# Kernel optimization log

Hardware: AMD Instinct MI355X
Metric: run time of the kernel (lower is better)

The kernel has to match this reference:

```python
import jax, jax.numpy as jnp
import numpy as np

N_COUNTRIES = 8
ADJ = jnp.array([
    [0, 1, 1, 1, 1, 1, 1, 0],
    [1, 0, 1, 0, 0, 0, 0, 1],
    [1, 1, 0, 1, 0, 1, 0, 0],
    [1, 0, 1, 0, 1, 1, 1, 0],
    [1, 0, 0, 1, 0, 1, 1, 0],
    [1, 0, 1, 1, 1, 0, 0, 0],
    [1, 0, 0, 1, 1, 0, 0, 0],
    [0, 1, 0, 0, 0, 0, 0, 0]], dtype=jnp.float32)
GDP = jnp.array([0.4, 0.15, 0.12, 0.1, 0.08, 0.08, 0.05, 0.02], dtype=jnp.float32)

B, D_IN, H, NH, L = 8192, 512, 256, 4, 3
HD = H * NH  # 1024: QKV width (no head reshape in the original)


def layer_norm(x, g, b, eps=1e-5):
    m = x.mean(-1, keepdims=True)
    v = ((x - m) ** 2).mean(-1, keepdims=True)
    return (x - m) * jax.lax.rsqrt(v + eps) * g + b


def setup_inputs() -> dict:
    key = jax.random.key(0)
    ks = jax.random.split(key, 12)
    lin = lambda k, i, o: (jax.random.normal(k, (i, o), jnp.float32) / np.sqrt(i).astype(np.float32))
    lin3 = lambda k, i, o: (jax.random.normal(k, (L, i, o), jnp.float32) / np.sqrt(i).astype(np.float32))
    return {
        'regional_features': jax.random.normal(ks[0], (B, D_IN), jnp.float32),
        'Wi': lin(ks[1], D_IN, H), 'bi': jnp.zeros((H,), jnp.float32),
        'emb': 0.02 * jax.random.normal(ks[2], (N_COUNTRIES, H), jnp.float32),
        'Wq': lin3(ks[3], H, HD), 'bq': jnp.zeros((L, HD), jnp.float32),
        'Wk': lin3(ks[4], H, HD), 'bk': jnp.zeros((L, HD), jnp.float32),
        'Wv': lin3(ks[5], H, HD), 'bv': jnp.zeros((L, HD), jnp.float32),
        'Wo': lin3(ks[6], HD, H), 'bo': jnp.zeros((L, H), jnp.float32),
        'ln_g': jnp.ones((L, H), jnp.float32), 'ln_b': jnp.zeros((L, H), jnp.float32),
        'Wp': lin(ks[7], H, H), 'bp': jnp.zeros((H,), jnp.float32),
        'lnp_g': jnp.ones((H,), jnp.float32), 'lnp_b': jnp.zeros((H,), jnp.float32),
    }


def reference(regional_features, Wi, bi, emb, Wq, bq, Wk, bk, Wv, bv, Wo, bo,
              ln_g, ln_b, Wp, bp, lnp_g, lnp_b):
    # input projection + broadcast over the 8 countries + country embedding
    h = regional_features @ Wi + bi                     # [B, H]
    x = h[:, None, :] + emb[None, :, :]                 # [B, 8, H]
    scale = 1.0 / np.sqrt(H).astype(np.float32)         # sqrt(dim)=sqrt(256), as in original
    mask = ADJ == 0                                     # [8, 8]
    for l in range(L):
        Q = x @ Wq[l] + bq[l]                           # [B, 8, HD]
        K = x @ Wk[l] + bk[l]
        V = x @ Wv[l] + bv[l]
        scores = jnp.einsum('bnd,bmd->bnm', Q, K) * scale  # [B, 8, 8]
        scores = jnp.where(mask[None], -jnp.inf, scores)
        attn = jax.nn.softmax(scores, axis=-1)          # dropout is identity in eval
        out = jnp.einsum('bnm,bmd->bnd', attn, V)       # [B, 8, HD]
        out = out @ Wo[l] + bo[l]                       # [B, 8, H]
        x = layer_norm(x + out, ln_g[l], ln_b[l])
    regional = jnp.sum(x * GDP[None, :, None], axis=1)  # [B, H]
    p = layer_norm(regional @ Wp + bp, lnp_g, lnp_b)
    return jax.nn.gelu(p, approximate=False)            # torch nn.GELU default = exact erf
```

## Files before the change

kernel.cpp:

```cpp
#include <hip/hip_runtime.h>
#include <hip/hip_bf16.h>
#include <math.h>


typedef short bf16x8 __attribute__((ext_vector_type(8)));
typedef float f32x4  __attribute__((ext_vector_type(4)));

__device__ __forceinline__ float bflo(unsigned int u){ return __uint_as_float(u << 16); }
__device__ __forceinline__ float bfhi(unsigned int u){ return __uint_as_float(u & 0xffff0000u); }
__device__ __forceinline__ float bfs(short s){ return __uint_as_float((unsigned int)(unsigned short)s << 16); }
__device__ __forceinline__ unsigned short f2bf(float f){
  __hip_bfloat16 h = __float2bfloat16(f);
  return *reinterpret_cast<unsigned short*>(&h);
}
__device__ __forceinline__ int gsw(int r, int q){ return (r + 16*q) ^ (r >> 2); }
__device__ __forceinline__ void unpack8(uint4 a, float* o){
  o[0]=bflo(a.x); o[1]=bfhi(a.x); o[2]=bflo(a.y); o[3]=bfhi(a.y);
  o[4]=bflo(a.z); o[5]=bfhi(a.z); o[6]=bflo(a.w); o[7]=bfhi(a.w);
}
__device__ __forceinline__ uint4 pack8(const float* v){
  uint4 r;
  r.x = (unsigned int)f2bf(v[0]) | ((unsigned int)f2bf(v[1]) << 16);
  r.y = (unsigned int)f2bf(v[2]) | ((unsigned int)f2bf(v[3]) << 16);
  r.z = (unsigned int)f2bf(v[4]) | ((unsigned int)f2bf(v[5]) << 16);
  r.w = (unsigned int)f2bf(v[6]) | ((unsigned int)f2bf(v[7]) << 16);
  return r;
}
__device__ __forceinline__ void gload16(const void* g, void* l){
  __builtin_amdgcn_global_load_lds(
      (const __attribute__((address_space(1))) unsigned int*)g,
      (__attribute__((address_space(3))) unsigned int*)l, 16, 0, 0);
}
__device__ __forceinline__ bf16x8 shfl8(bf16x8 v, int src){
  union U { bf16x8 h; int u[4]; };
  U a, r; a.h = v;
  #pragma unroll
  for (int j = 0; j < 4; j++) r.u[j] = __shfl(a.u[j], src);
  return r.h;
}
__device__ __forceinline__ bf16x8 pk8(const float* v){
  bf16x8 r;
  #pragma unroll
  for (int j = 0; j < 8; j++) r[j] = (short)f2bf(v[j]);
  return r;
}

struct CvP { const float* src[4]; short* dst[4]; int boff[5]; };
__global__ __launch_bounds__(256) void k_convert(CvP p){
  int bid = blockIdx.x, s = 0;
  while (bid >= p.boff[s+1]) s++;
  size_t e = (size_t)(bid - p.boff[s]) * 2048 + (size_t)threadIdx.x * 8;
  const float* src = p.src[s] + e;
  float4 v0 = *(const float4*)src;
  float4 v1 = *(const float4*)(src + 4);
  float v[8] = {v0.x,v0.y,v0.z,v0.w,v1.x,v1.y,v1.z,v1.w};
  *(uint4*)(p.dst[s] + e) = pack8(v);
}

struct TrP { const float* src[5]; short* dst[5]; int rows[5]; int cols[5]; int toff[6]; };
__global__ __launch_bounds__(256) void k_transpose(TrP p){
  __shared__ float tile[64][65];
  int bid = blockIdx.x, s = 0;
  while (bid >= p.toff[s+1]) s++;
  int ti = bid - p.toff[s];
  int cols = p.cols[s], rows = p.rows[s];
  int ntc = cols >> 6;
  int r0 = (ti / ntc) * 64, c0 = (ti % ntc) * 64;
  const float* src = p.src[s];
  int row = threadIdx.x >> 2, jb = (threadIdx.x & 3) * 16;
  #pragma unroll
  for (int j = 0; j < 16; j += 4){
    float4 v = *(const float4*)(src + (size_t)(r0 + row) * cols + c0 + jb + j);
    tile[row][jb+j] = v.x; tile[row][jb+j+1] = v.y; tile[row][jb+j+2] = v.z; tile[row][jb+j+3] = v.w;
  }
  __syncthreads();
  short* dst = p.dst[s];
  float tmp[16];
  #pragma unroll
  for (int j = 0; j < 16; j++) tmp[j] = tile[jb + j][row];
  #pragma unroll
  for (int j = 0; j < 16; j += 8)
    *(uint4*)(dst + (size_t)(c0 + row) * rows + r0 + jb + j) = pack8(&tmp[j]);
}

__global__ __launch_bounds__(256) void k_vecs2(
    const short* Wqb, const short* Wkb, const short* WoTb,
    const float* bq, const float* bk, const float* bv, const float* bo,
    float* cq, float* ck, float* cvo, float* c0){
  const int job = blockIdx.x, l = blockIdx.y, tid = threadIdx.x;
  __shared__ float sv[1024];
  __shared__ float red[256];
  if (job == 3){
    float pp = 0.f;
    #pragma unroll
    for (int i = 0; i < 4; i++){
      int d = tid*4 + i;
      pp = fmaf(bq[l*1024 + d], bk[l*1024 + d], pp);
    }
    red[tid] = pp; __syncthreads();
    for (int o = 128; o > 0; o >>= 1){ if (tid < o) red[tid] += red[tid + o]; __syncthreads(); }
    if (tid == 0) c0[l] = red[0] * 0.0625f;
    return;
  }
  const short* rows = (job==0 ? Wqb : job==1 ? Wkb : WoTb) + (size_t)l*262144;
  const float* vecg = (job==0 ? bk : job==1 ? bq : bv) + l*1024;
  const float scale = (job == 2) ? 1.0f : 0.0625f;
  for (int i = tid; i < 1024; i += 256) sv[i] = vecg[i];
  __syncthreads();
  const int row = tid >> 3, sub = tid & 7;
  for (int pass = 0; pass < 8; pass++){
    int r = pass*32 + row;
    const short* rp = rows + (size_t)r*1024;
    float acc = 0.f;
    #pragma unroll
    for (int i = 0; i < 16; i++){
      int d = sub*8 + i*64;
      uint4 v = *(const uint4*)(rp + d);
      float f[8]; unpack8(v, f);
      #pragma unroll
      for (int j = 0; j < 8; j++) acc = fmaf(f[j], sv[d + j], acc);
    }
    acc += __shfl_xor(acc, 1); acc += __shfl_xor(acc, 2); acc += __shfl_xor(acc, 4);
    if (sub == 0){
      float o = acc * scale;
      if (job == 2) o += bo[l*256 + r];
      (job==0 ? cq : job==1 ? ck : cvo)[l*256 + r] = o;
    }
  }
}

struct GDesc { const short* A; const short* Bt; short* C; int K; float scale; };
struct GemmP { GDesc d[6]; };
__global__ __launch_bounds__(256) void k_gemm128(GemmP p){
  GDesc g = p.d[blockIdx.z];
  const int tid = threadIdx.x, lane = tid & 63, w = tid >> 6;
  const int wm = w >> 1, wn = w & 1;
  __shared__ alignas(16) short As[128*32];
  __shared__ alignas(16) short Bs[128*32];
  const int K = g.K;
  const short* Ab = g.A + (size_t)blockIdx.x * 128 * K;
  const short* Bb = g.Bt + (size_t)blockIdx.y * 128 * K;
  f32x4 acc[4][4] = {};
  for (int k0 = 0; k0 < K; k0 += 32){
    #pragma unroll
    for (int i = 0; i < 2; i++){
      int s = w*2 + i;
      int ro = (s >> 2)*64 + (s & 3)*16 + (lane & 15);
      int co = k0 + (lane >> 4) * 8;
      gload16(Ab + (size_t)ro * K + co, &As[s*512]);
      gload16(Bb + (size_t)ro * K + co, &Bs[s*512]);
    }
    __syncthreads();
    bf16x8 av[4], bv[4];
    #pragma unroll
    for (int mi = 0; mi < 4; mi++)
      av[mi] = *(const bf16x8*)&As[((wm*4 + mi)*64 + lane)*8];
    #pragma unroll
    for (int nj = 0; nj < 4; nj++)
      bv[nj] = *(const bf16x8*)&Bs[((wn*4 + nj)*64 + lane)*8];
    #pragma unroll
    for (int mi = 0; mi < 4; mi++)
      #pragma unroll
      for (int nj = 0; nj < 4; nj++)
        acc[mi][nj] = __builtin_amdgcn_mfma_f32_16x16x32_bf16(av[mi], bv[nj], acc[mi][nj], 0, 0, 0);
    __syncthreads();
  }
  const int ldc = gridDim.y * 128;
  #pragma unroll
  for (int mi = 0; mi < 4; mi++)
    #pragma unroll
    for (int nj = 0; nj < 4; nj++){
      int rm0 = blockIdx.x*128 + wm*64 + mi*16 + (lane >> 4) * 4;
      int cn  = blockIdx.y*128 + wn*64 + nj*16 + (lane & 15);
      #pragma unroll
      for (int j = 0; j < 4; j++)
        g.C[(size_t)(rm0 + j) * ldc + cn] = (short)f2bf(acc[mi][nj][j] * g.scale);
    }
}

struct RpP { const short* src[8]; short* dst[8]; int K[8]; int boff[9]; };
__global__ __launch_bounds__(256) void k_repack(RpP p){
  int bid = blockIdx.x, s = 0;
  while (bid >= p.boff[s+1]) s++;
  int kk = bid - p.boff[s];
  const short* src = p.src[s];
  short* dst = p.dst[s] + (size_t)kk * 8192;
  int K = p.K[s];
  int r15 = threadIdx.x & 15, nt = threadIdx.x >> 4;
  const short* sp = src + (size_t)(nt*16 + r15) * K + kk*32;
  short* dp = dst + nt*512 + r15*8;
  #pragma unroll
  for (int q = 0; q < 4; q++)
    *(uint4*)(dp + q*128) = *(const uint4*)(sp + q*8);
}

__global__ __launch_bounds__(512, 2) void k_net(
    const float* __restrict__ rf, const short* __restrict__ WiT,
    const float* __restrict__ bi, const float* __restrict__ emb,
    const short* __restrict__ Wqk, const short* __restrict__ Wvo,
    const float* __restrict__ ckv, const float* __restrict__ cvov,
    const float* __restrict__ lng, const float* __restrict__ lnb,
    const short* __restrict__ WpT, const float* __restrict__ bpv,
    const float* __restrict__ lpg, const float* __restrict__ lpb,
    float* __restrict__ outp){
  const int tid = threadIdx.x, lane = tid & 63, w = tid >> 6;
  const int b0 = blockIdx.x * 16;
  const int dsub = (lane >> 4) * 8;
  const int glane = gsw(lane & 15, lane >> 4);
  __shared__ alignas(16) short tst[8][4096];
  __shared__ alignas(16) short wbuf[32768];
  __shared__ alignas(16) float atn[8][16][16];
  __shared__ short ckb[256];
  __shared__ float s_add[256], s_g[256], s_b[256];
  __shared__ float redS[8][16], redQ[8][16], s_mean[16], s_rstd[16];

  #define LKW  asm volatile("s_waitcnt lgkmcnt(0)" ::: "memory")
  #define VMW0 asm volatile("s_waitcnt vmcnt(0)" ::: "memory")

  auto STAGEW = [&](const short* W, int h){
    #pragma unroll
    for (int i = 0; i < 8; i++)
      gload16(W + (size_t)(w*16 + h*8 + i)*512 + lane*8, &wbuf[(w*8 + i)*512]);
  };

  float* hst  = (float*)&tst[0][0];
  float* embs = hst + 16*264;
  float* bis  = embs + 2048;
  if (tid < 256) bis[tid] = bi[tid];
  for (int i = tid; i < 2048; i += 512) embs[i] = emb[i];
  f32x4 hacc[2] = {};
  #pragma unroll
  for (int kk = 0; kk < 16; kk++){
    const float* ap = rf + (size_t)(b0 + (lane & 15)) * 512 + kk*32 + dsub;
    float4 a0 = *(const float4*)ap, a1 = *(const float4*)(ap + 4);
    float af[8] = {a0.x,a0.y,a0.z,a0.w,a1.x,a1.y,a1.z,a1.w};
    bf16x8 av = pk8(af);
    #pragma unroll
    for (int nj = 0; nj < 2; nj++){
      bf16x8 bv = *(const bf16x8*)(WiT + (size_t)(kk*16 + w*2 + nj)*512 + lane*8);
      hacc[nj] = __builtin_amdgcn_mfma_f32_16x16x32_bf16(av, bv, hacc[nj], 0, 0, 0);
    }
  }
  __syncthreads();
  #pragma unroll
  for (int nj = 0; nj < 2; nj++)
    #pragma unroll
    for (int jj = 0; jj < 4; jj++){
      int m = (lane >> 4)*4 + jj, col = w*32 + nj*16 + (lane & 15);
      hst[m*264 + col] = hacc[nj][jj] + bis[col];
    }
  __syncthreads();
  bf16x8 xf[8];
  {
    int r15 = lane & 15;
    int bt = w*2 + (r15 >> 3), ct = r15 & 7;
    #pragma unroll
    for (int c = 0; c < 8; c++){
      float v8[8];
      #pragma unroll
      for (int e = 0; e < 8; e++){
        int d = dsub + 32*c + e;
        v8[e] = hst[bt*264 + d] + embs[ct*256 + d];
      }
      xf[c] = pk8(v8);
    }
  }

  const unsigned long long MASK64 = 0x02191D69752B857EULL;

  #pragma unroll 1
  for (int l = 0; l < 3; ++l){
    __syncthreads();
    if (tid < 256){
      ckb[tid]   = (short)f2bf(ckv[l*256 + tid]);
      s_add[tid] = cvov[l*256 + tid];
      s_g[tid]   = lng[l*256 + tid];
      s_b[tid]   = lnb[l*256 + tid];
    }
    const short* Wq_ = Wqk + l*65536;
    const short* Wv_ = Wvo + l*65536;
    STAGEW(Wq_, 0);
    VMW0; __syncthreads();

    f32x4 sacc = {0.f, 0.f, 0.f, 0.f};
    #pragma unroll
    for (int h = 0; h < 2; h++){
      f32x4 acc[8] = {};
      #pragma unroll
      for (int kk = 0; kk < 8; kk++)
        #pragma unroll
        for (int nj = 0; nj < 8; nj++){
          bf16x8 bv = *(const bf16x8*)&wbuf[(kk*8 + nj)*512 + lane*8];
          acc[nj] = __builtin_amdgcn_mfma_f32_16x16x32_bf16(xf[kk], bv, acc[nj], 0, 0, 0);
        }
      if (h == 0){ __syncthreads(); STAGEW(Wq_, 1); }
      #pragma unroll
      for (int nj = 0; nj < 8; nj++)
        #pragma unroll
        for (int jj = 0; jj < 4; jj++){
          int i_ = (lane >> 4)*4 + jj, nl = nj*16 + (lane & 15);
          tst[w][(nl >> 5)*512 + gsw(i_, (nl >> 3) & 3)*8 + (nl & 7)] = (short)f2bf(acc[nj][jj]);
        }
      LKW; __builtin_amdgcn_sched_barrier(0);
      #pragma unroll
      for (int cl = 0; cl < 4; cl++){
        bf16x8 tf = *(const bf16x8*)&tst[w][cl*512 + glane*8];
        sacc = __builtin_amdgcn_mfma_f32_16x16x32_bf16(tf, xf[h*4 + cl], sacc, 0, 0, 0);
      }
      LKW;
      if (h == 0){ VMW0; __syncthreads(); }
    }
    __syncthreads();
    STAGEW(Wv_, 0);

    float skv = 0.f;
    #pragma unroll
    for (int c = 0; c < 8; c++){
      bf16x8 cv = *(const bf16x8*)&ckb[c*32 + dsub];
      #pragma unroll
      for (int e = 0; e < 8; e++) skv = fmaf(bfs(xf[c][e]), bfs(cv[e]), skv);
    }
    skv += __shfl_xor(skv, 16); skv += __shfl_xor(skv, 32);

    #pragma unroll
    for (int jj = 0; jj < 4; jj++){
      int i_ = (lane >> 4)*4 + jj, j_ = lane & 15;
      bool ok = (((i_ ^ j_) & 8) == 0) &&
                ((MASK64 >> (((i_ & 7) << 3) | (j_ & 7))) & 1ull);
      float sv = ok ? (sacc[jj] + skv) : -3.0e38f;
      float mx = sv;
      mx = fmaxf(mx, __shfl_xor(mx, 1));
      mx = fmaxf(mx, __shfl_xor(mx, 2));
      mx = fmaxf(mx, __shfl_xor(mx, 4));
      float e = ok ? __expf(sv - mx) : 0.f;
      float sum = e;
      sum += __shfl_xor(sum, 1); sum += __shfl_xor(sum, 2); sum += __shfl_xor(sum, 4);
      atn[w][i_][j_] = e / sum;
    }
    LKW;

    bf16x8 yfrag[8];
    {
      float4 A0 = *(const float4*)&atn[w][lane & 15][lane & 8];
      float4 A1 = *(const float4*)&atn[w][lane & 15][(lane & 8) + 4];
      float am[8] = {A0.x, A0.y, A0.z, A0.w, A1.x, A1.y, A1.z, A1.w};
      #pragma unroll
      for (int c = 0; c < 8; c++){
        float a8[8] = {0,0,0,0,0,0,0,0};
        #pragma unroll
        for (int mi = 0; mi < 8; mi++){
          bf16x8 xs = shfl8(xf[c], (lane & 48) | (lane & 8) | mi);
          #pragma unroll
          for (int e = 0; e < 8; e++) a8[e] = fmaf(am[mi], bfs(xs[e]), a8[e]);
        }
        yfrag[c] = pk8(a8);
      }
    }
    VMW0; __syncthreads();

    float rs = 0.f, rq = 0.f;
    float* fst = (float*)&tst[w][0];
    #pragma unroll
    for (int h = 0; h < 2; h++){
      f32x4 acc[8] = {};
      #pragma unroll
      for (int kk = 0; kk < 8; kk++)
        #pragma unroll
        for (int nj = 0; nj < 8; nj++){
          bf16x8 bv = *(const bf16x8*)&wbuf[(kk*8 + nj)*512 + lane*8];
          acc[nj] = __builtin_amdgcn_mfma_f32_16x16x32_bf16(yfrag[kk], bv, acc[nj], 0, 0, 0);
        }
      if (h == 0){ __syncthreads(); STAGEW(Wv_, 1); }
      #pragma unroll
      for (int nj = 0; nj < 8; nj++)
        #pragma unroll
        for (int jj = 0; jj < 4; jj++){
          int i_ = (lane >> 4)*4 + jj;
          int dq = nj*16 + (lane & 15);
          fst[(dq >> 5)*512 + gsw(i_, (dq >> 3) & 3)*8 + (dq & 7)] = acc[nj][jj];
        }
      LKW; __builtin_amdgcn_sched_barrier(0);
      #pragma unroll
      for (int lc = 0; lc < 4; lc++){
        int c = h*4 + lc;
        float v8[8];
        #pragma unroll
        for (int e = 0; e < 8; e++){
          int d = 32*c + dsub + e;
          float t = fst[lc*512 + glane*8 + e] + s_add[d] + bfs(xf[c][e]);
          rs += t; rq = fmaf(t, t, rq);
          v8[e] = t;
        }
        xf[c] = pk8(v8);
      }
      LKW;
      if (h == 0){ VMW0; __syncthreads(); }
    }
    rs += __shfl_xor(rs, 16); rs += __shfl_xor(rs, 32);
    rq += __shfl_xor(rq, 16); rq += __shfl_xor(rq, 32);
    float mn = rs * (1.f/256.f);
    float var = rq * (1.f/256.f) - mn*mn;
    float rr = rsqrtf(fmaxf(var, 0.f) + 1e-5f);
    #pragma unroll
    for (int c = 0; c < 8; c++){
      float v8[8];
      #pragma unroll
      for (int e = 0; e < 8; e++){
        int d = 32*c + dsub + e;
        v8[e] = (bfs(xf[c][e]) - mn) * rr * s_g[d] + s_b[d];
      }
      xf[c] = pk8(v8);
    }
  }

  __syncthreads();
  short* Ast = &tst[0][0];
  {
    int c7 = lane & 7;
    float g = (c7 == 0) ? 0.4f : (c7 == 1) ? 0.15f : (c7 == 2) ? 0.12f :
              (c7 == 3) ? 0.1f : (c7 == 4) ? 0.08f : (c7 == 5) ? 0.08f :
              (c7 == 6) ? 0.05f : 0.02f;
    #pragma unroll
    for (int c = 0; c < 8; c++){
      float v8[8];
      #pragma unroll
      for (int e = 0; e < 8; e++){
        float v = g * bfs(xf[c][e]);
        v += __shfl_xor(v, 1); v += __shfl_xor(v, 2); v += __shfl_xor(v, 4);
        v8[e] = v;
      }
      if ((lane & 7) == 0){
        int bt = w*2 + ((lane >> 3) & 1);
        *(bf16x8*)&Ast[bt*264 + dsub + 32*c] = pk8(v8);
      }
    }
  }
  __syncthreads();
  f32x4 ha[2] = {};
  #pragma unroll
  for (int kk = 0; kk < 8; kk++){
    bf16x8 av = *(const bf16x8*)&Ast[(lane & 15)*264 + kk*32 + dsub];
    #pragma unroll
    for (int nj = 0; nj < 2; nj++){
      bf16x8 bv = *(const bf16x8*)(WpT + (size_t)(kk*16 + w*2 + nj)*512 + lane*8);
      ha[nj] = __builtin_amdgcn_mfma_f32_16x16x32_bf16(av, bv, ha[nj], 0, 0, 0);
    }
  }
  #pragma unroll
  for (int jj = 0; jj < 4; jj++){
    float s = 0.f, q = 0.f;
    #pragma unroll
    for (int nj = 0; nj < 2; nj++){
      int cx = w*32 + nj*16 + (lane & 15);
      float t = ha[nj][jj] + bpv[cx];
      ha[nj][jj] = t;
      s += t; q = fmaf(t, t, q);
    }
    s += __shfl_xor(s, 1); q += __shfl_xor(q, 1);
    s += __shfl_xor(s, 2); q += __shfl_xor(q, 2);
    s += __shfl_xor(s, 4); q += __shfl_xor(q, 4);
    s += __shfl_xor(s, 8); q += __shfl_xor(q, 8);
    if ((lane & 15) == 0){
      int rl = (lane >> 4)*4 + jj;
      redS[w][rl] = s; redQ[w][rl] = q;
    }
  }
  __syncthreads();
  if (tid < 16){
    float sm = 0.f, sq = 0.f;
    #pragma unroll
    for (int w2 = 0; w2 < 8; w2++){ sm += redS[w2][tid]; sq += redQ[w2][tid]; }
    float mn = sm * (1.f/256.f);
    float var = sq * (1.f/256.f) - mn*mn;
    s_mean[tid] = mn;
    s_rstd[tid] = rsqrtf(fmaxf(var, 0.f) + 1e-5f);
  }
  __syncthreads();
  #pragma unroll
  for (int jj = 0; jj < 4; jj++){
    int rl = (lane >> 4)*4 + jj;
    float mn = s_mean[rl], rstd = s_rstd[rl];
    #pragma unroll
    for (int nj = 0; nj < 2; nj++){
      int cx = w*32 + nj*16 + (lane & 15);
      float y = (ha[nj][jj] - mn) * rstd * lpg[cx] + lpb[cx];
      outp[(size_t)(b0 + rl)*256 + cx] = 0.5f * y * (1.0f + erff(y * 0.70710678118654752f));
    }
  }
  #undef LKW
  #undef VMW0
}

extern "C" void kernel_launch(void* const* d_in, const int* in_sizes, int n_in,
                              void* d_out, int out_size, void* d_ws, size_t ws_size,
                              hipStream_t stream){
  (void)in_sizes; (void)n_in; (void)out_size; (void)ws_size;
  const float* rf  = (const float*)d_in[0];
  const float* Wi  = (const float*)d_in[1];
  const float* bi  = (const float*)d_in[2];
  const float* emb = (const float*)d_in[3];
  const float* Wq  = (const float*)d_in[4];
  const float* bq  = (const float*)d_in[5];
  const float* Wk  = (const float*)d_in[6];
  const float* bk  = (const float*)d_in[7];
  const float* Wv  = (const float*)d_in[8];
  const float* bv  = (const float*)d_in[9];
  const float* Wo  = (const float*)d_in[10];
  const float* bo  = (const float*)d_in[11];
  const float* lng = (const float*)d_in[12];
  const float* lnb = (const float*)d_in[13];
  const float* Wp  = (const float*)d_in[14];
  const float* bp  = (const float*)d_in[15];
  const float* lpg = (const float*)d_in[16];
  const float* lpb = (const float*)d_in[17];

  char* ws = (char*)d_ws;
  short* Wqb  = (short*)(ws);
  short* Wkb  = (short*)(ws + 1572864ull);
  short* Wvb  = (short*)(ws + 3145728ull);
  short* WoTb = (short*)(ws + 4718592ull);
  short* WiTb = (short*)(ws + 6291456ull);
  short* WpTb = (short*)(ws + 6553600ull);
  short* Wqk  = (short*)(ws + 6684672ull);
  short* Wvo  = (short*)(ws + 7077888ull);
  float* cqv  = (float*)(ws + 7471104ull);
  float* ckv  = (float*)(ws + 7474176ull);
  float* cvov = (float*)(ws + 7477248ull);
  float* c0v  = (float*)(ws + 7480320ull);
  short* WqkP = (short*)(ws + 7483392ull);
  short* WvoP = (short*)(ws + 7876608ull);
  short* WiTP = (short*)(ws + 8269824ull);
  short* WpTP = (short*)(ws + 8531968ull);

  { CvP cv;
    cv.src[0]=Wq; cv.dst[0]=Wqb;
    cv.src[1]=Wk; cv.dst[1]=Wkb;
    cv.src[2]=Wv; cv.dst[2]=Wvb;
    cv.src[3]=Wv; cv.dst[3]=Wvb;
    cv.boff[0]=0; cv.boff[1]=384; cv.boff[2]=768; cv.boff[3]=1152; cv.boff[4]=1152;
    k_convert<<<dim3(1152), dim3(256), 0, stream>>>(cv); }

  { TrP tp;
    tp.src[0]=Wi;          tp.dst[0]=WiTb;          tp.rows[0]=512;  tp.cols[0]=256;
    tp.src[1]=Wo;          tp.dst[1]=WoTb;          tp.rows[1]=1024; tp.cols[1]=256;
    tp.src[2]=Wo+262144;   tp.dst[2]=WoTb+262144;   tp.rows[2]=1024; tp.cols[2]=256;
    tp.src[3]=Wo+524288;   tp.dst[3]=WoTb+524288;   tp.rows[3]=1024; tp.cols[3]=256;
    tp.src[4]=Wp;          tp.dst[4]=WpTb;          tp.rows[4]=256;  tp.cols[4]=256;
    tp.toff[0]=0; tp.toff[1]=32; tp.toff[2]=96; tp.toff[3]=160; tp.toff[4]=224; tp.toff[5]=240;
    k_transpose<<<dim3(240), dim3(256), 0, stream>>>(tp); }

  k_vecs2<<<dim3(4, 3), dim3(256), 0, stream>>>(Wqb, Wkb, WoTb, bq, bk, bv, bo,
                                                cqv, ckv, cvov, c0v);

  { GemmP g{};
    for (int l = 0; l < 3; l++){
      g.d[l]   = GDesc{ Wkb  + l*262144, Wqb + l*262144, Wqk + l*65536, 1024, 0.0625f };
      g.d[3+l] = GDesc{ WoTb + l*262144, Wvb + l*262144, Wvo + l*65536, 1024, 1.0f };
    }
    k_gemm128<<<dim3(2,2,6), dim3(256), 0, stream>>>(g); }

  { RpP rp;
    for (int l = 0; l < 3; l++){
      rp.src[l]   = Wqk + l*65536; rp.dst[l]   = WqkP + l*65536; rp.K[l]   = 256;
      rp.src[3+l] = Wvo + l*65536; rp.dst[3+l] = WvoP + l*65536; rp.K[3+l] = 256;
    }
    rp.src[6] = WiTb; rp.dst[6] = WiTP; rp.K[6] = 512;
    rp.src[7] = WpTb; rp.dst[7] = WpTP; rp.K[7] = 256;
    rp.boff[0]=0; rp.boff[1]=8; rp.boff[2]=16; rp.boff[3]=24; rp.boff[4]=32;
    rp.boff[5]=40; rp.boff[6]=48; rp.boff[7]=64; rp.boff[8]=72;
    k_repack<<<dim3(72), dim3(256), 0, stream>>>(rp); }

  k_net<<<dim3(512), dim3(512), 0, stream>>>(rf, WiTP, bi, emb, WqkP, WvoP,
      ckv, cvov, lng, lnb, WpTP, bp, lpg, lpb, (float*)d_out);
}
```

Baseline: 255.6 us.

## Merge weight-prep kernels into two launches with packed-layout writes

Folds the convert and transpose kernels into one prep launch. Folds the weight-product GEMMs and bias-vector reductions into a second launch that uses 64x64 tiles across 96 blocks. The GEMM and transpose epilogues now write straight into the MFMA-packed layout, so the separate repack kernel goes away, and the unused cq/c0 vectors are no longer computed. This removes three launches and one intermediate round trip through memory. The cost is scattered 2-byte stores in the GEMM epilogue and uneven work across blocks in the merged kernels.

```diff
diff --git a/kernel.cpp b/kernel.cpp
--- a/kernel.cpp
+++ b/kernel.cpp
@@ -44,29 +44,35 @@
   for (int j = 0; j < 8; j++) r[j] = (short)f2bf(v[j]);
   return r;
 }
-
-struct CvP { const float* src[4]; short* dst[4]; int boff[5]; };
-__global__ __launch_bounds__(256) void k_convert(CvP p){
-  int bid = blockIdx.x, s = 0;
-  while (bid >= p.boff[s+1]) s++;
-  size_t e = (size_t)(bid - p.boff[s]) * 2048 + (size_t)threadIdx.x * 8;
-  const float* src = p.src[s] + e;
-  float4 v0 = *(const float4*)src;
-  float4 v1 = *(const float4*)(src + 4);
-  float v[8] = {v0.x,v0.y,v0.z,v0.w,v1.x,v1.y,v1.z,v1.w};
-  *(uint4*)(p.dst[s] + e) = pack8(v);
-}
-
-struct TrP { const float* src[5]; short* dst[5]; int rows[5]; int cols[5]; int toff[6]; };
-__global__ __launch_bounds__(256) void k_transpose(TrP p){
+__device__ __forceinline__ int pidx(int n, int k){
+  return (k >> 5)*8192 + (n >> 4)*512 + ((k >> 3) & 3)*128 + (n & 15)*8 + (k & 7);
+}
+
+struct P1P {
+  const float* csrc[3]; short* cdst[3];
+  const float* tsrc[5]; short* tdst[5];
+  int trows[5]; int tcols[5]; int tpack[5]; int toff[6];
+};
+__global__ __launch_bounds__(256) void k_prep1(P1P p){
   __shared__ float tile[64][65];
-  int bid = blockIdx.x, s = 0;
-  while (bid >= p.toff[s+1]) s++;
-  int ti = bid - p.toff[s];
-  int cols = p.cols[s], rows = p.rows[s];
+  int bid = blockIdx.x;
+  if (bid < 1152){
+    int s = bid / 384, lb = bid % 384;
+    size_t e = (size_t)lb * 2048 + (size_t)threadIdx.x * 8;
+    const float* src = p.csrc[s] + e;
+    float4 v0 = *(const float4*)src;
+    float4 v1 = *(const float4*)(src + 4);
+    float v[8] = {v0.x,v0.y,v0.z,v0.w,v1.x,v1.y,v1.z,v1.w};
+    *(uint4*)(p.cdst[s] + e) = pack8(v);
+    return;
+  }
+  int tb = bid - 1152, s = 0;
+  while (tb >= p.toff[s+1]) s++;
+  int ti = tb - p.toff[s];
+  int cols = p.tcols[s], rows = p.trows[s];
   int ntc = cols >> 6;
   int r0 = (ti / ntc) * 64, c0 = (ti % ntc) * 64;
-  const float* src = p.src[s];
+  const float* src = p.tsrc[s];
   int row = threadIdx.x >> 2, jb = (threadIdx.x & 3) * 16;
   #pragma unroll
   for (int j = 0; j < 16; j += 4){
@@ -74,38 +80,87 @@
     tile[row][jb+j] = v.x; tile[row][jb+j+1] = v.y; tile[row][jb+j+2] = v.z; tile[row][jb+j+3] = v.w;
   }
   __syncthreads();
-  short* dst = p.dst[s];
+  short* dst = p.tdst[s];
   float tmp[16];
   #pragma unroll
   for (int j = 0; j < 16; j++) tmp[j] = tile[jb + j][row];
-  #pragma unroll
-  for (int j = 0; j < 16; j += 8)
-    *(uint4*)(dst + (size_t)(c0 + row) * rows + r0 + jb + j) = pack8(&tmp[j]);
-}
-
-__global__ __launch_bounds__(256) void k_vecs2(
-    const short* Wqb, const short* Wkb, const short* WoTb,
-    const float* bq, const float* bk, const float* bv, const float* bo,
-    float* cq, float* ck, float* cvo, float* c0){
-  const int job = blockIdx.x, l = blockIdx.y, tid = threadIdx.x;
+  if (p.tpack[s]){
+    int n = c0 + row;
+    #pragma unroll
+    for (int gq = 0; gq < 2; gq++){
+      int k = r0 + jb + gq*8;
+      *(uint4*)(dst + pidx(n, k)) = pack8(&tmp[gq*8]);
+    }
+  } else {
+    #pragma unroll
+    for (int j = 0; j < 16; j += 8)
+      *(uint4*)(dst + (size_t)(c0 + row) * rows + r0 + jb + j) = pack8(&tmp[j]);
+  }
+}
+
+struct GD2 { const short* A; const short* Bt; short* Cp; float scale; };
+struct P2P {
+  GD2 d[6];
+  const short* Wkb; const short* WoTb;
+  const float* bq; const float* bv; const float* bo;
+  float* ck; float* cvo;
+};
+__global__ __launch_bounds__(256) void k_prep2(P2P p){
+  __shared__ alignas(16) short As[64*128];
+  __shared__ alignas(16) short Bs[64*128];
   __shared__ float sv[1024];
-  __shared__ float red[256];
-  if (job == 3){
-    float pp = 0.f;
-    #pragma unroll
-    for (int i = 0; i < 4; i++){
-      int d = tid*4 + i;
-      pp = fmaf(bq[l*1024 + d], bk[l*1024 + d], pp);
-    }
-    red[tid] = pp; __syncthreads();
-    for (int o = 128; o > 0; o >>= 1){ if (tid < o) red[tid] += red[tid + o]; __syncthreads(); }
-    if (tid == 0) c0[l] = red[0] * 0.0625f;
+  const int bid = blockIdx.x, tid = threadIdx.x;
+  if (bid < 96){
+    const int lane = tid & 63, w = tid >> 6;
+    const int wm = w >> 1, wn = w & 1;
+    const int z = bid >> 4, rem = bid & 15, bx = rem >> 2, by = rem & 3;
+    GD2 g = p.d[z];
+    const int K = 1024;
+    f32x4 acc[2][2] = {};
+    for (int k0 = 0; k0 < K; k0 += 128){
+      #pragma unroll
+      for (int kc = 0; kc < 4; kc++){
+        int ro = w*16 + (lane & 15);
+        int co = k0 + kc*32 + (lane >> 4)*8;
+        gload16(g.A  + (size_t)(bx*64 + ro)*K + co, &As[(kc*4 + w)*512]);
+        gload16(g.Bt + (size_t)(by*64 + ro)*K + co, &Bs[(kc*4 + w)*512]);
+      }
+      __syncthreads();
+      #pragma unroll
+      for (int kc = 0; kc < 4; kc++){
+        bf16x8 av[2], bv[2];
+        #pragma unroll
+        for (int mi = 0; mi < 2; mi++)
+          av[mi] = *(const bf16x8*)&As[((kc*4 + wm*2 + mi)*64 + lane)*8];
+        #pragma unroll
+        for (int nj = 0; nj < 2; nj++)
+          bv[nj] = *(const bf16x8*)&Bs[((kc*4 + wn*2 + nj)*64 + lane)*8];
+        #pragma unroll
+        for (int mi = 0; mi < 2; mi++)
+          #pragma unroll
+          for (int nj = 0; nj < 2; nj++)
+            acc[mi][nj] = __builtin_amdgcn_mfma_f32_16x16x32_bf16(av[mi], bv[nj], acc[mi][nj], 0, 0, 0);
+      }
+      __syncthreads();
+    }
+    #pragma unroll
+    for (int mi = 0; mi < 2; mi++)
+      #pragma unroll
+      for (int nj = 0; nj < 2; nj++)
+        #pragma unroll
+        for (int j = 0; j < 4; j++){
+          int r = bx*64 + wm*32 + mi*16 + (lane >> 4)*4 + j;
+          int c = by*64 + wn*32 + nj*16 + (lane & 15);
+          g.Cp[pidx(r, c)] = (short)f2bf(acc[mi][nj][j] * g.scale);
+        }
     return;
   }
-  const short* rows = (job==0 ? Wqb : job==1 ? Wkb : WoTb) + (size_t)l*262144;
-  const float* vecg = (job==0 ? bk : job==1 ? bq : bv) + l*1024;
-  const float scale = (job == 2) ? 1.0f : 0.0625f;
-  for (int i = tid; i < 1024; i += 256) sv[i] = vecg[i];
+  int v = bid - 96;
+  int job = v / 3, l = v % 3;
+  const short* rows = (job == 0 ? p.Wkb : p.WoTb) + (size_t)l*262144;
+  const float* vec  = (job == 0 ? p.bq : p.bv) + l*1024;
+  const float scale = (job == 0) ? 0.0625f : 1.0f;
+  for (int i = tid; i < 1024; i += 256) sv[i] = vec[i];
   __syncthreads();
   const int row = tid >> 3, sub = tid & 7;
   for (int pass = 0; pass < 8; pass++){
@@ -115,83 +170,18 @@
     #pragma unroll
     for (int i = 0; i < 16; i++){
       int d = sub*8 + i*64;
-      uint4 v = *(const uint4*)(rp + d);
-      float f[8]; unpack8(v, f);
+      uint4 vv = *(const uint4*)(rp + d);
+      float f[8]; unpack8(vv, f);
       #pragma unroll
       for (int j = 0; j < 8; j++) acc = fmaf(f[j], sv[d + j], acc);
     }
     acc += __shfl_xor(acc, 1); acc += __shfl_xor(acc, 2); acc += __shfl_xor(acc, 4);
     if (sub == 0){
       float o = acc * scale;
-      if (job == 2) o += bo[l*256 + r];
-      (job==0 ? cq : job==1 ? ck : cvo)[l*256 + r] = o;
-    }
-  }
-}
-
-struct GDesc { const short* A; const short* Bt; short* C; int K; float scale; };
-struct GemmP { GDesc d[6]; };
-__global__ __launch_bounds__(256) void k_gemm128(GemmP p){
-  GDesc g = p.d[blockIdx.z];
-  const int tid = threadIdx.x, lane = tid & 63, w = tid >> 6;
-  const int wm = w >> 1, wn = w & 1;
-  __shared__ alignas(16) short As[128*32];
-  __shared__ alignas(16) short Bs[128*32];
-  const int K = g.K;
-  const short* Ab = g.A + (size_t)blockIdx.x * 128 * K;
-  const short* Bb = g.Bt + (size_t)blockIdx.y * 128 * K;
-  f32x4 acc[4][4] = {};
-  for (int k0 = 0; k0 < K; k0 += 32){
-    #pragma unroll
-    for (int i = 0; i < 2; i++){
-      int s = w*2 + i;
-      int ro = (s >> 2)*64 + (s & 3)*16 + (lane & 15);
-      int co = k0 + (lane >> 4) * 8;
-      gload16(Ab + (size_t)ro * K + co, &As[s*512]);
-      gload16(Bb + (size_t)ro * K + co, &Bs[s*512]);
-    }
-    __syncthreads();
-    bf16x8 av[4], bv[4];
-    #pragma unroll
-    for (int mi = 0; mi < 4; mi++)
-      av[mi] = *(const bf16x8*)&As[((wm*4 + mi)*64 + lane)*8];
-    #pragma unroll
-    for (int nj = 0; nj < 4; nj++)
-      bv[nj] = *(const bf16x8*)&Bs[((wn*4 + nj)*64 + lane)*8];
-    #pragma unroll
-    for (int mi = 0; mi < 4; mi++)
-      #pragma unroll
-      for (int nj = 0; nj < 4; nj++)
-        acc[mi][nj] = __builtin_amdgcn_mfma_f32_16x16x32_bf16(av[mi], bv[nj], acc[mi][nj], 0, 0, 0);
-    __syncthreads();
-  }
-  const int ldc = gridDim.y * 128;
-  #pragma unroll
-  for (int mi = 0; mi < 4; mi++)
-    #pragma unroll
-    for (int nj = 0; nj < 4; nj++){
-      int rm0 = blockIdx.x*128 + wm*64 + mi*16 + (lane >> 4) * 4;
-      int cn  = blockIdx.y*128 + wn*64 + nj*16 + (lane & 15);
-      #pragma unroll
-      for (int j = 0; j < 4; j++)
-        g.C[(size_t)(rm0 + j) * ldc + cn] = (short)f2bf(acc[mi][nj][j] * g.scale);
-    }
-}
-
-struct RpP { const short* src[8]; short* dst[8]; int K[8]; int boff[9]; };
-__global__ __launch_bounds__(256) void k_repack(RpP p){
-  int bid = blockIdx.x, s = 0;
-  while (bid >= p.boff[s+1]) s++;
-  int kk = bid - p.boff[s];
-  const short* src = p.src[s];
-  short* dst = p.dst[s] + (size_t)kk * 8192;
-  int K = p.K[s];
-  int r15 = threadIdx.x & 15, nt = threadIdx.x >> 4;
-  const short* sp = src + (size_t)(nt*16 + r15) * K + kk*32;
-  short* dp = dst + nt*512 + r15*8;
-  #pragma unroll
-  for (int q = 0; q < 4; q++)
-    *(uint4*)(dp + q*128) = *(const uint4*)(sp + q*8);
+      if (job == 1) o += p.bo[l*256 + r];
+      (job == 0 ? p.ck : p.cvo)[l*256 + r] = o;
+    }
+  }
 }
 
 __global__ __launch_bounds__(512, 2) void k_net(
@@ -513,62 +503,41 @@
   const float* bp  = (const float*)d_in[15];
   const float* lpg = (const float*)d_in[16];
   const float* lpb = (const float*)d_in[17];
+  (void)bk;
 
   char* ws = (char*)d_ws;
   short* Wqb  = (short*)(ws);
   short* Wkb  = (short*)(ws + 1572864ull);
   short* Wvb  = (short*)(ws + 3145728ull);
   short* WoTb = (short*)(ws + 4718592ull);
-  short* WiTb = (short*)(ws + 6291456ull);
-  short* WpTb = (short*)(ws + 6553600ull);
-  short* Wqk  = (short*)(ws + 6684672ull);
-  short* Wvo  = (short*)(ws + 7077888ull);
-  float* cqv  = (float*)(ws + 7471104ull);
-  float* ckv  = (float*)(ws + 7474176ull);
-  float* cvov = (float*)(ws + 7477248ull);
-  float* c0v  = (float*)(ws + 7480320ull);
-  short* WqkP = (short*)(ws + 7483392ull);
-  short* WvoP = (short*)(ws + 7876608ull);
-  short* WiTP = (short*)(ws + 8269824ull);
-  short* WpTP = (short*)(ws + 8531968ull);
-
-  { CvP cv;
-    cv.src[0]=Wq; cv.dst[0]=Wqb;
-    cv.src[1]=Wk; cv.dst[1]=Wkb;
-    cv.src[2]=Wv; cv.dst[2]=Wvb;
-    cv.src[3]=Wv; cv.dst[3]=Wvb;
-    cv.boff[0]=0; cv.boff[1]=384; cv.boff[2]=768; cv.boff[3]=1152; cv.boff[4]=1152;
-    k_convert<<<dim3(1152), dim3(256), 0, stream>>>(cv); }
-
-  { TrP tp;
-    tp.src[0]=Wi;          tp.dst[0]=WiTb;          tp.rows[0]=512;  tp.cols[0]=256;
-    tp.src[1]=Wo;          tp.dst[1]=WoTb;          tp.rows[1]=1024; tp.cols[1]=256;
-    tp.src[2]=Wo+262144;   tp.dst[2]=WoTb+262144;   tp.rows[2]=1024; tp.cols[2]=256;
-    tp.src[3]=Wo+524288;   tp.dst[3]=WoTb+524288;   tp.rows[3]=1024; tp.cols[3]=256;
-    tp.src[4]=Wp;          tp.dst[4]=WpTb;          tp.rows[4]=256;  tp.cols[4]=256;
-    tp.toff[0]=0; tp.toff[1]=32; tp.toff[2]=96; tp.toff[3]=160; tp.toff[4]=224; tp.toff[5]=240;
-    k_transpose<<<dim3(240), dim3(256), 0, stream>>>(tp); }
-
-  k_vecs2<<<dim3(4, 3), dim3(256), 0, stream>>>(Wqb, Wkb, WoTb, bq, bk, bv, bo,
-                                                cqv, ckv, cvov, c0v);
-
-  { GemmP g{};
+  short* WqkP = (short*)(ws + 6291456ull);
+  short* WvoP = (short*)(ws + 6684672ull);
+  short* WiTP = (short*)(ws + 7077888ull);
+  short* WpTP = (short*)(ws + 7340032ull);
+  float* ckv  = (float*)(ws + 7471104ull);
+  float* cvov = (float*)(ws + 7474176ull);
+
+  { P1P p;
+    p.csrc[0]=Wq; p.cdst[0]=Wqb;
+    p.csrc[1]=Wk; p.cdst[1]=Wkb;
+    p.csrc[2]=Wv; p.cdst[2]=Wvb;
+    p.tsrc[0]=Wi;        p.tdst[0]=WiTP;          p.trows[0]=512;  p.tcols[0]=256; p.tpack[0]=1;
+    p.tsrc[1]=Wo;        p.tdst[1]=WoTb;          p.trows[1]=1024; p.tcols[1]=256; p.tpack[1]=0;
+    p.tsrc[2]=Wo+262144; p.tdst[2]=WoTb+262144;   p.trows[2]=1024; p.tcols[2]=256; p.tpack[2]=0;
+    p.tsrc[3]=Wo+524288; p.tdst[3]=WoTb+524288;   p.trows[3]=1024; p.tcols[3]=256; p.tpack[3]=0;
+    p.tsrc[4]=Wp;        p.tdst[4]=WpTP;          p.trows[4]=256;  p.tcols[4]=256; p.tpack[4]=1;
+    p.toff[0]=0; p.toff[1]=32; p.toff[2]=96; p.toff[3]=160; p.toff[4]=224; p.toff[5]=240;
+    k_prep1<<<dim3(1392), dim3(256), 0, stream>>>(p); }
+
+  { P2P p;
     for (int l = 0; l < 3; l++){
-      g.d[l]   = GDesc{ Wkb  + l*262144, Wqb + l*262144, Wqk + l*65536, 1024, 0.0625f };
-      g.d[3+l] = GDesc{ WoTb + l*262144, Wvb + l*262144, Wvo + l*65536, 1024, 1.0f };
-    }
-    k_gemm128<<<dim3(2,2,6), dim3(256), 0, stream>>>(g); }
-
-  { RpP rp;
-    for (int l = 0; l < 3; l++){
-      rp.src[l]   = Wqk + l*65536; rp.dst[l]   = WqkP + l*65536; rp.K[l]   = 256;
-      rp.src[3+l] = Wvo + l*65536; rp.dst[3+l] = WvoP + l*65536; rp.K[3+l] = 256;
-    }
-    rp.src[6] = WiTb; rp.dst[6] = WiTP; rp.K[6] = 512;
-    rp.src[7] = WpTb; rp.dst[7] = WpTP; rp.K[7] = 256;
-    rp.boff[0]=0; rp.boff[1]=8; rp.boff[2]=16; rp.boff[3]=24; rp.boff[4]=32;
-    rp.boff[5]=40; rp.boff[6]=48; rp.boff[7]=64; rp.boff[8]=72;
-    k_repack<<<dim3(72), dim3(256), 0, stream>>>(rp); }
+      p.d[l]   = GD2{ Wkb  + l*262144, Wqb + l*262144, WqkP + l*65536, 0.0625f };
+      p.d[3+l] = GD2{ WoTb + l*262144, Wvb + l*262144, WvoP + l*65536, 1.0f };
+    }
+    p.Wkb = Wkb; p.WoTb = WoTb;
+    p.bq = bq; p.bv = bv; p.bo = bo;
+    p.ck = ckv; p.cvo = cvov;
+    k_prep2<<<dim3(102), dim3(256), 0, stream>>>(p); }
 
   k_net<<<dim3(512), dim3(512), 0, stream>>>(rf, WiTP, bi, emb, WqkP, WvoP,
       ckv, cvov, lng, lnb, WpTP, bp, lpg, lpb, (float*)d_out);
```

After: 206.4 us. 1.24x faster.
